# Optimization experiments

Hardware: AMD Instinct MI355X
Metric: run time of the kernel (lower is better)

The kernel has to match this reference:

```python
import jax, jax.numpy as jnp
import numpy as np

# PQMatcher forward (cleaned): per passage timestep i, additive (Bahdanau-style)
# attention over all question positions:
#   x = tanh(Wp(Up[i]) + Wq(Uq) + Wv(v));  s = x . v;  a = softmax(s over lq)
#   c[i] = a @ Uq
# The original python loop over i is loop-invariant except Wp(Up[i]), so it
# vectorizes exactly into one broadcasted tanh + einsum. (The original also
# computed a duplicate s_/a_ from Upr==Up and Uqr==Uq which is identical math
# and unused; we compute it once.)

LP, LQ, BZ, SZ, H = 400, 50, 32, 768, 128


def setup_inputs() -> dict:
    key = jax.random.key(0)
    ks = jax.random.split(key, 9)
    s_in = 1.0 / np.sqrt(SZ)
    s_h = 1.0 / np.sqrt(H)
    return {
        "Up": jax.random.normal(ks[0], (LP, BZ, SZ), jnp.float32),
        "Uq": jax.random.normal(ks[1], (LQ, BZ, SZ), jnp.float32),
        "Wp_w": jax.random.normal(ks[2], (H, SZ), jnp.float32) * s_in,
        "Wp_b": jax.random.normal(ks[3], (H,), jnp.float32) * s_in,
        "Wq_w": jax.random.normal(ks[4], (H, SZ), jnp.float32) * s_in,
        "Wq_b": jax.random.normal(ks[5], (H,), jnp.float32) * s_in,
        "Wv_w": jax.random.normal(ks[6], (H, H), jnp.float32) * s_h,
        "Wv_b": jax.random.normal(ks[7], (H,), jnp.float32) * s_h,
        "v": jax.random.normal(ks[8], (BZ, H), jnp.float32),
    }


def reference(Up, Uq, Wp_w, Wp_b, Wq_w, Wq_b, Wv_w, Wv_b, v):
    # Projections (loop-invariant parts hoisted out of the original loop)
    Wup = jnp.einsum("pbs,hs->pbh", Up, Wp_w) + Wp_b  # [lp, bz, h]
    Wuq = jnp.einsum("qbs,hs->qbh", Uq, Wq_w) + Wq_b  # [lq, bz, h]
    Wvv = jnp.einsum("bh,gh->bg", v, Wv_w) + Wv_b      # [bz, h]
    # tanh score fusion: [lp, lq, bz, h]
    x = jnp.tanh(Wup[:, None, :, :] + Wuq[None, :, :, :] + Wvv[None, None, :, :])
    # scores s[i] = x[i] . v  -> [lp, bz, lq]
    s = jnp.einsum("pqbh,bh->pbq", x, v)
    a = jax.nn.softmax(s, axis=-1)                      # softmax over question len
    # contexts c[i] = a[i] @ Uq -> [lp, bz, sz]
    c = jnp.einsum("pbq,qbs->pbs", a, Uq)
    return c
```

## Files before the change

### kernel.cpp

```cpp
#include <hip/hip_runtime.h>

#define LP 400
#define LQ 50
#define BZ 32
#define SZ 768
#define HH 128
#define PR_TOT 14400

typedef unsigned short u16;
typedef __attribute__((ext_vector_type(8))) short short8;
typedef __attribute__((ext_vector_type(4))) float f32x4;

__device__ __forceinline__ float fexp2(float x) {
#if __has_builtin(__builtin_amdgcn_exp2f)
  return __builtin_amdgcn_exp2f(x);
#else
  return exp2f(x);
#endif
}
__device__ __forceinline__ float frcp(float x) {
#if __has_builtin(__builtin_amdgcn_rcpf)
  return __builtin_amdgcn_rcpf(x);
#else
  return 1.0f / x;
#endif
}

__device__ __forceinline__ unsigned pack2(float x, float y) {
  return (__float_as_uint(x) >> 16) | (__float_as_uint(y) & 0xffff0000u);
}
__device__ __forceinline__ float remf(float x) {
  return x - __uint_as_float(__float_as_uint(x) & 0xffff0000u);
}

__global__ __launch_bounds__(256) void prep_kernel(
    const float* __restrict__ Wp_w, const float* __restrict__ Wq_w,
    const float* __restrict__ v, const float* __restrict__ Wv_w,
    const float* __restrict__ Wv_b,
    u16* __restrict__ Wph, u16* __restrict__ Wpl,
    u16* __restrict__ Wqh, u16* __restrict__ Wql, float* __restrict__ Wvv) {
  const int bx = blockIdx.x, t = threadIdx.x;
  if (bx < 96) {
    int gid = bx * 256 + t;
    int base = gid * 8;
    const float* src;
    u16 *dh, *dl;
    if (base < HH * SZ) {
      src = Wp_w + base; dh = Wph + base; dl = Wpl + base;
    } else {
      int o = base - HH * SZ;
      src = Wq_w + o; dh = Wqh + o; dl = Wql + o;
    }
    float4 x0 = *(const float4*)src;
    float4 x1 = *(const float4*)(src + 4);
    uint4 H, L;
    H.x = pack2(x0.x, x0.y); H.y = pack2(x0.z, x0.w);
    H.z = pack2(x1.x, x1.y); H.w = pack2(x1.z, x1.w);
    L.x = pack2(remf(x0.x), remf(x0.y)); L.y = pack2(remf(x0.z), remf(x0.w));
    L.z = pack2(remf(x1.x), remf(x1.y)); L.w = pack2(remf(x1.z), remf(x1.w));
    *(uint4*)dh = H;
    *(uint4*)dl = L;
  } else {
    int id = (bx - 96) * 256 + t;
    int b = id >> 7, g = id & 127;
    const float4* vb = reinterpret_cast<const float4*>(v + b * HH);
    const float4* wr = reinterpret_cast<const float4*>(Wv_w + g * HH);
    float s = Wv_b[g];
#pragma unroll
    for (int i = 0; i < HH / 4; ++i) {
      float4 a = vb[i], w = wr[i];
      s = fmaf(a.x, w.x, s); s = fmaf(a.y, w.y, s);
      s = fmaf(a.z, w.z, s); s = fmaf(a.w, w.w, s);
    }
    Wvv[id] = s;
  }
}

__global__ __launch_bounds__(256, 2) void mfma_gemm(
    const float* __restrict__ Up, const float* __restrict__ Uq,
    const u16* __restrict__ Wph, const u16* __restrict__ Wpl,
    const u16* __restrict__ Wqh, const u16* __restrict__ Wql,
    float* __restrict__ partial) {
  __shared__ u16 Ah[64][40], Al[64][40], Bh[128][40], Bl[128][40];
  const int t = threadIdx.x, lane = t & 63, wid = t >> 6;
  const int bx = blockIdx.x, z = blockIdx.y;
  const int m0 = bx * 64;
  const bool probq = (bx >= 200);
  const u16* WH = probq ? Wqh : Wph;
  const u16* WL = probq ? Wql : Wpl;
  const int k0base = z * 384;

  const int ra = t >> 1, kh = (t & 1) * 16;
  const bool hasA = (ra < 64);
  const int grow = m0 + (ra & 63);
  const float* srcA = (grow < 12800) ? (Up + (size_t)grow * SZ)
                                     : (Uq + (size_t)(grow - 12800) * SZ);
  const u16* srcWH = WH + ra * SZ;
  const u16* srcWL = WL + ra * SZ;

  const int wm = (wid >> 1) * 32, wn = (wid & 1) * 64;
  const int fr = lane & 15, fg = lane >> 4;

  f32x4 acc[2][4];
#pragma unroll
  for (int i = 0; i < 2; ++i)
#pragma unroll
    for (int j = 0; j < 4; ++j) acc[i][j] = (f32x4){0.f, 0.f, 0.f, 0.f};

  float4 a0, a1, a2, a3;
  uint4 wh0, wh1, wl0, wl1;

#define GLOAD(s)                                                         \
  do {                                                                   \
    int kk = k0base + (s) * 32 + kh;                                     \
    if (hasA) {                                                          \
      a0 = *(const float4*)(srcA + kk);                                  \
      a1 = *(const float4*)(srcA + kk + 4);                              \
      a2 = *(const float4*)(srcA + kk + 8);                              \
      a3 = *(const float4*)(srcA + kk + 12);                             \
    }                                                                    \
    wh0 = *(const uint4*)(srcWH + kk); wh1 = *(const uint4*)(srcWH + kk + 8); \
    wl0 = *(const uint4*)(srcWL + kk); wl1 = *(const uint4*)(srcWL + kk + 8); \
  } while (0)

#define WSTORE()                                                          \
  do {                                                                    \
    if (hasA) {                                                           \
      uint4 H0, H1, L0, L1;                                               \
      H0.x = pack2(a0.x, a0.y); H0.y = pack2(a0.z, a0.w);                 \
      H0.z = pack2(a1.x, a1.y); H0.w = pack2(a1.z, a1.w);                 \
      H1.x = pack2(a2.x, a2.y); H1.y = pack2(a2.z, a2.w);                 \
      H1.z = pack2(a3.x, a3.y); H1.w = pack2(a3.z, a3.w);                 \
      L0.x = pack2(remf(a0.x), remf(a0.y)); L0.y = pack2(remf(a0.z), remf(a0.w)); \
      L0.z = pack2(remf(a1.x), remf(a1.y)); L0.w = pack2(remf(a1.z), remf(a1.w)); \
      L1.x = pack2(remf(a2.x), remf(a2.y)); L1.y = pack2(remf(a2.z), remf(a2.w)); \
      L1.z = pack2(remf(a3.x), remf(a3.y)); L1.w = pack2(remf(a3.z), remf(a3.w)); \
      *(uint4*)&Ah[ra][kh] = H0; *(uint4*)&Ah[ra][kh + 8] = H1;           \
      *(uint4*)&Al[ra][kh] = L0; *(uint4*)&Al[ra][kh + 8] = L1;           \
    }                                                                     \
    *(uint4*)&Bh[ra][kh] = wh0; *(uint4*)&Bh[ra][kh + 8] = wh1;           \
    *(uint4*)&Bl[ra][kh] = wl0; *(uint4*)&Bl[ra][kh + 8] = wl1;           \
  } while (0)

  GLOAD(0);
  WSTORE();
  __syncthreads();

  for (int s = 0; s < 12; ++s) {
    if (s < 11) GLOAD(s + 1);
    short8 ah[2], al[2], bh[4], bl[4];
#pragma unroll
    for (int i = 0; i < 2; ++i) {
      ah[i] = *(const short8*)&Ah[wm + i * 16 + fr][fg * 8];
      al[i] = *(const short8*)&Al[wm + i * 16 + fr][fg * 8];
    }
#pragma unroll
    for (int j = 0; j < 4; ++j) {
      bh[j] = *(const short8*)&Bh[wn + j * 16 + fr][fg * 8];
      bl[j] = *(const short8*)&Bl[wn + j * 16 + fr][fg * 8];
    }
#pragma unroll
    for (int i = 0; i < 2; ++i)
#pragma unroll
      for (int j = 0; j < 4; ++j) {
        acc[i][j] = __builtin_amdgcn_mfma_f32_16x16x32_bf16(ah[i], bh[j], acc[i][j], 0, 0, 0);
        acc[i][j] = __builtin_amdgcn_mfma_f32_16x16x32_bf16(ah[i], bl[j], acc[i][j], 0, 0, 0);
        acc[i][j] = __builtin_amdgcn_mfma_f32_16x16x32_bf16(al[i], bh[j], acc[i][j], 0, 0, 0);
      }
    __syncthreads();
    if (s < 11) WSTORE();
    __syncthreads();
  }
#undef GLOAD
#undef WSTORE

  float* pz = partial + (size_t)z * (PR_TOT * HH);
#pragma unroll
  for (int i = 0; i < 2; ++i) {
    int r0 = m0 + wm + i * 16 + fg * 4;
#pragma unroll
    for (int j = 0; j < 4; ++j) {
      int c = wn + j * 16 + fr;
#pragma unroll
      for (int e = 0; e < 4; ++e) pz[(size_t)(r0 + e) * HH + c] = acc[i][j][e];
    }
  }
}

__global__ __launch_bounds__(256, 4) void score_ctx(
    const float* __restrict__ partial, const float* __restrict__ Wp_b,
    const float* __restrict__ Wq_b, const float* __restrict__ Wvv,
    const float* __restrict__ v, const float* __restrict__ Uq,
    float* __restrict__ out, float TS) {
  const int f = blockIdx.x;
  const int b = ((f & 7) << 2) | ((f >> 3) & 3);
  const int pbase = (f >> 5) * 8;
  const int t = threadIdx.x, lane = t & 63, w = t >> 6;
  __shared__ float W2s[HH][52];
  __shared__ f32x4 Wps4[8][32];
  __shared__ f32x4 vsh4[32];
  __shared__ float as_[8][52];

  for (int ff = t; ff < LQ * 32; ff += 256) {
    int q_ = ff % LQ, c4 = ff / LQ;
    size_t row = 12800 + (size_t)(q_ * BZ + b);
    float4 p0 = *(const float4*)&partial[row * HH + c4 * 4];
    float4 p1 = *(const float4*)&partial[((size_t)PR_TOT + row) * HH + c4 * 4];
    float4 bb = *(const float4*)&Wq_b[c4 * 4];
    float4 wv = *(const float4*)&Wvv[b * HH + c4 * 4];
    W2s[c4 * 4 + 0][q_] = (p0.x + p1.x + bb.x + wv.x) * TS;
    W2s[c4 * 4 + 1][q_] = (p0.y + p1.y + bb.y + wv.y) * TS;
    W2s[c4 * 4 + 2][q_] = (p0.z + p1.z + bb.z + wv.z) * TS;
    W2s[c4 * 4 + 3][q_] = (p0.w + p1.w + bb.w + wv.w) * TS;
  }
  {
    int i = t >> 5, c4 = t & 31;
    size_t grow = (size_t)(pbase + i) * BZ + b;
    float4 p0 = *(const float4*)&partial[grow * HH + c4 * 4];
    float4 p1 = *(const float4*)&partial[((size_t)PR_TOT + grow) * HH + c4 * 4];
    float4 bb = *(const float4*)&Wp_b[c4 * 4];
    Wps4[i][c4] = (f32x4){(p0.x + p1.x + bb.x) * TS, (p0.y + p1.y + bb.y) * TS,
                          (p0.z + p1.z + bb.z) * TS, (p0.w + p1.w + bb.w) * TS};
  }
  if (t < 32) {
    float4 x = *(const float4*)&v[b * HH + t * 4];
    vsh4[t] = (f32x4){x.x, x.y, x.z, x.w};
  }
  __syncthreads();

  const int q = (lane < LQ) ? lane : (LQ - 1);
  const int prow = w * 2;
  float A0 = 0.f, A1 = 0.f;
  for (int h4 = 0; h4 < 32; ++h4) {
    f32x4 vj = vsh4[h4];
    f32x4 w0 = Wps4[prow][h4];
    f32x4 w1 = Wps4[prow + 1][h4];
    float s0 = W2s[h4 * 4 + 0][q];
    float s1 = W2s[h4 * 4 + 1][q];
    float s2 = W2s[h4 * 4 + 2][q];
    float s3 = W2s[h4 * 4 + 3][q];
    A0 = fmaf(vj[0], frcp(fexp2(w0[0] + s0) + 1.f), A0);
    A0 = fmaf(vj[1], frcp(fexp2(w0[1] + s1) + 1.f), A0);
    A0 = fmaf(vj[2], frcp(fexp2(w0[2] + s2) + 1.f), A0);
    A0 = fmaf(vj[3], frcp(fexp2(w0[3] + s3) + 1.f), A0);
    A1 = fmaf(vj[0], frcp(fexp2(w1[0] + s0) + 1.f), A1);
    A1 = fmaf(vj[1], frcp(fexp2(w1[1] + s1) + 1.f), A1);
    A1 = fmaf(vj[2], frcp(fexp2(w1[2] + s2) + 1.f), A1);
    A1 = fmaf(vj[3], frcp(fexp2(w1[3] + s3) + 1.f), A1);
  }

#define SOFTMAX(AR, PI)                                                   \
  do {                                                                    \
    float a = (lane < LQ) ? (AR) : 1e30f;                                 \
    float mn = a;                                                         \
    mn = fminf(mn, __shfl_xor(mn, 1));  mn = fminf(mn, __shfl_xor(mn, 2)); \
    mn = fminf(mn, __shfl_xor(mn, 4));  mn = fminf(mn, __shfl_xor(mn, 8)); \
    mn = fminf(mn, __shfl_xor(mn, 16)); mn = fminf(mn, __shfl_xor(mn, 32)); \
    float e = fexp2((mn - a) * TS);         \
    float sm = e;                                                         \
    sm += __shfl_xor(sm, 1);  sm += __shfl_xor(sm, 2);                    \
    sm += __shfl_xor(sm, 4);  sm += __shfl_xor(sm, 8);                    \
    sm += __shfl_xor(sm, 16); sm += __shfl_xor(sm, 32);                   \
    float val = e * frcp(sm);                                             \
    if (lane < LQ) as_[prow + (PI)][lane] = val;                          \
  } while (0)

  SOFTMAX(A0, 0); SOFTMAX(A1, 1);
#undef SOFTMAX
  __syncthreads();

  if (t < 192) {
    const int s4 = t * 4;
    f32x4 acc[8];
#pragma unroll
    for (int i = 0; i < 8; ++i) acc[i] = (f32x4){0.f, 0.f, 0.f, 0.f};
    for (int qp = 0; qp < LQ; qp += 2) {
      float4 u0 = *(const float4*)&Uq[(size_t)(qp * BZ + b) * SZ + s4];
      float4 u1 = *(const float4*)&Uq[(size_t)((qp + 1) * BZ + b) * SZ + s4];
#pragma unroll
      for (int i = 0; i < 8; ++i) {
        float2 a2 = *(const float2*)&as_[i][qp];
        acc[i][0] = fmaf(a2.x, u0.x, acc[i][0]); acc[i][1] = fmaf(a2.x, u0.y, acc[i][1]);
        acc[i][2] = fmaf(a2.x, u0.z, acc[i][2]); acc[i][3] = fmaf(a2.x, u0.w, acc[i][3]);
        acc[i][0] = fmaf(a2.y, u1.x, acc[i][0]); acc[i][1] = fmaf(a2.y, u1.y, acc[i][1]);
        acc[i][2] = fmaf(a2.y, u1.z, acc[i][2]); acc[i][3] = fmaf(a2.y, u1.w, acc[i][3]);
      }
    }
#pragma unroll
    for (int i = 0; i < 8; ++i) {
      float4 r = make_float4(acc[i][0], acc[i][1], acc[i][2], acc[i][3]);
      *(float4*)&out[(size_t)((pbase + i) * BZ + b) * SZ + s4] = r;
    }
  }
}

extern "C" void kernel_launch(void* const* d_in, const int* in_sizes, int n_in,
                              void* d_out, int out_size, void* d_ws, size_t ws_size,
                              hipStream_t stream) {
  const float* Up   = (const float*)d_in[0];
  const float* Uq   = (const float*)d_in[1];
  const float* Wp_w = (const float*)d_in[2];
  const float* Wp_b = (const float*)d_in[3];
  const float* Wq_w = (const float*)d_in[4];
  const float* Wq_b = (const float*)d_in[5];
  const float* Wv_w = (const float*)d_in[6];
  const float* Wv_b = (const float*)d_in[7];
  const float* v    = (const float*)d_in[8];
  float* out = (float*)d_out;

  float* ws      = (float*)d_ws;
  float* Wvv     = ws;
  u16* Wph       = (u16*)(Wvv + BZ * HH);
  u16* Wpl       = Wph + HH * SZ;
  u16* Wqh       = Wpl + HH * SZ;
  u16* Wql       = Wqh + HH * SZ;
  float* partial = (float*)(Wql + HH * SZ);

  const float TS = 2.8853900817779268f;

  prep_kernel<<<dim3(112), dim3(256), 0, stream>>>(
      Wp_w, Wq_w, v, Wv_w, Wv_b, Wph, Wpl, Wqh, Wql, Wvv);
  mfma_gemm<<<dim3(225, 2), dim3(256), 0, stream>>>(
      Up, Uq, Wph, Wpl, Wqh, Wql, partial);
  score_ctx<<<dim3(1600), dim3(256), 0, stream>>>(
      partial, Wp_b, Wq_b, Wvv, v, Uq, out, TS);
}
```

Baseline: 174.3 us.

## Split GEMM K four ways and separate score and context kernels

Raises the split-K factor of the projection GEMM from 2 to 4, so twice as many blocks each run half as many K steps. The fused score/context kernel is split into a score+softmax kernel that writes attention weights to workspace and a separate 192-thread context kernel. Each block now handles 16 passage rows instead of 8, with a b-major mapping chosen per XCD to improve reuse of the Uq and partial rows. In exchange it writes and reads twice as many partial sums, adds a global round trip for the attention weights, and costs one more kernel launch.

Result: slower. 313.1 us (+79.7%).

```diff
diff --git a/kernel.cpp b/kernel.cpp
--- a/kernel.cpp
+++ b/kernel.cpp
@@ -6,6 +6,7 @@
 #define SZ 768
 #define HH 128
 #define PR_TOT 14400
+#define NZ 4
 
 typedef unsigned short u16;
 typedef __attribute__((ext_vector_type(8))) short short8;
@@ -88,7 +89,7 @@
   const bool probq = (bx >= 200);
   const u16* WH = probq ? Wqh : Wph;
   const u16* WL = probq ? Wql : Wpl;
-  const int k0base = z * 384;
+  const int k0base = z * 192;
 
   const int ra = t >> 1, kh = (t & 1) * 16;
   const bool hasA = (ra < 64);
@@ -146,8 +147,8 @@
   WSTORE();
   __syncthreads();
 
-  for (int s = 0; s < 12; ++s) {
-    if (s < 11) GLOAD(s + 1);
+  for (int s = 0; s < 6; ++s) {
+    if (s < 5) GLOAD(s + 1);
     short8 ah[2], al[2], bh[4], bl[4];
 #pragma unroll
     for (int i = 0; i < 2; ++i) {
@@ -168,7 +169,7 @@
         acc[i][j] = __builtin_amdgcn_mfma_f32_16x16x32_bf16(al[i], bh[j], acc[i][j], 0, 0, 0);
       }
     __syncthreads();
-    if (s < 11) WSTORE();
+    if (s < 5) WSTORE();
     __syncthreads();
   }
 #undef GLOAD
@@ -187,40 +188,49 @@
   }
 }
 
-__global__ __launch_bounds__(256, 4) void score_ctx(
+__global__ __launch_bounds__(256, 4) void score_kernel(
     const float* __restrict__ partial, const float* __restrict__ Wp_b,
     const float* __restrict__ Wq_b, const float* __restrict__ Wvv,
-    const float* __restrict__ v, const float* __restrict__ Uq,
-    float* __restrict__ out, float TS) {
+    const float* __restrict__ v, float* __restrict__ aw, float TS) {
   const int f = blockIdx.x;
-  const int b = ((f & 7) << 2) | ((f >> 3) & 3);
-  const int pbase = (f >> 5) * 8;
+  const int xcd = f & 7, j = f >> 3;
+  const int b = xcd * 4 + j / 25;
+  const int pbase = (j % 25) * 16;
   const int t = threadIdx.x, lane = t & 63, w = t >> 6;
   __shared__ float W2s[HH][52];
-  __shared__ f32x4 Wps4[8][32];
+  __shared__ f32x4 Wps4[16][32];
   __shared__ f32x4 vsh4[32];
-  __shared__ float as_[8][52];
 
   for (int ff = t; ff < LQ * 32; ff += 256) {
     int q_ = ff % LQ, c4 = ff / LQ;
     size_t row = 12800 + (size_t)(q_ * BZ + b);
-    float4 p0 = *(const float4*)&partial[row * HH + c4 * 4];
-    float4 p1 = *(const float4*)&partial[((size_t)PR_TOT + row) * HH + c4 * 4];
+    const float* pp = &partial[row * HH + c4 * 4];
+    float4 p0 = *(const float4*)pp;
+    float4 p1 = *(const float4*)(pp + (size_t)PR_TOT * HH);
+    float4 p2 = *(const float4*)(pp + (size_t)2 * PR_TOT * HH);
+    float4 p3 = *(const float4*)(pp + (size_t)3 * PR_TOT * HH);
     float4 bb = *(const float4*)&Wq_b[c4 * 4];
     float4 wv = *(const float4*)&Wvv[b * HH + c4 * 4];
-    W2s[c4 * 4 + 0][q_] = (p0.x + p1.x + bb.x + wv.x) * TS;
-    W2s[c4 * 4 + 1][q_] = (p0.y + p1.y + bb.y + wv.y) * TS;
-    W2s[c4 * 4 + 2][q_] = (p0.z + p1.z + bb.z + wv.z) * TS;
-    W2s[c4 * 4 + 3][q_] = (p0.w + p1.w + bb.w + wv.w) * TS;
-  }
-  {
-    int i = t >> 5, c4 = t & 31;
+    W2s[c4 * 4 + 0][q_] = (p0.x + p1.x + p2.x + p3.x + bb.x + wv.x) * TS;
+    W2s[c4 * 4 + 1][q_] = (p0.y + p1.y + p2.y + p3.y + bb.y + wv.y) * TS;
+    W2s[c4 * 4 + 2][q_] = (p0.z + p1.z + p2.z + p3.z + bb.z + wv.z) * TS;
+    W2s[c4 * 4 + 3][q_] = (p0.w + p1.w + p2.w + p3.w + bb.w + wv.w) * TS;
+  }
+#pragma unroll
+  for (int rep = 0; rep < 2; ++rep) {
+    int ff = t + rep * 256;
+    int i = ff >> 5, c4 = ff & 31;
     size_t grow = (size_t)(pbase + i) * BZ + b;
-    float4 p0 = *(const float4*)&partial[grow * HH + c4 * 4];
-    float4 p1 = *(const float4*)&partial[((size_t)PR_TOT + grow) * HH + c4 * 4];
+    const float* pp = &partial[grow * HH + c4 * 4];
+    float4 p0 = *(const float4*)pp;
+    float4 p1 = *(const float4*)(pp + (size_t)PR_TOT * HH);
+    float4 p2 = *(const float4*)(pp + (size_t)2 * PR_TOT * HH);
+    float4 p3 = *(const float4*)(pp + (size_t)3 * PR_TOT * HH);
     float4 bb = *(const float4*)&Wp_b[c4 * 4];
-    Wps4[i][c4] = (f32x4){(p0.x + p1.x + bb.x) * TS, (p0.y + p1.y + bb.y) * TS,
-                          (p0.z + p1.z + bb.z) * TS, (p0.w + p1.w + bb.w) * TS};
+    Wps4[i][c4] = (f32x4){(p0.x + p1.x + p2.x + p3.x + bb.x) * TS,
+                          (p0.y + p1.y + p2.y + p3.y + bb.y) * TS,
+                          (p0.z + p1.z + p2.z + p3.z + bb.z) * TS,
+                          (p0.w + p1.w + p2.w + p3.w + bb.w) * TS};
   }
   if (t < 32) {
     float4 x = *(const float4*)&v[b * HH + t * 4];
@@ -229,12 +239,14 @@
   __syncthreads();
 
   const int q = (lane < LQ) ? lane : (LQ - 1);
-  const int prow = w * 2;
-  float A0 = 0.f, A1 = 0.f;
+  const int prow = w * 4;
+  float A0 = 0.f, A1 = 0.f, A2 = 0.f, A3 = 0.f;
   for (int h4 = 0; h4 < 32; ++h4) {
     f32x4 vj = vsh4[h4];
-    f32x4 w0 = Wps4[prow][h4];
+    f32x4 w0 = Wps4[prow + 0][h4];
     f32x4 w1 = Wps4[prow + 1][h4];
+    f32x4 w2 = Wps4[prow + 2][h4];
+    f32x4 w3 = Wps4[prow + 3][h4];
     float s0 = W2s[h4 * 4 + 0][q];
     float s1 = W2s[h4 * 4 + 1][q];
     float s2 = W2s[h4 * 4 + 2][q];
@@ -247,6 +259,14 @@
     A1 = fmaf(vj[1], frcp(fexp2(w1[1] + s1) + 1.f), A1);
     A1 = fmaf(vj[2], frcp(fexp2(w1[2] + s2) + 1.f), A1);
     A1 = fmaf(vj[3], frcp(fexp2(w1[3] + s3) + 1.f), A1);
+    A2 = fmaf(vj[0], frcp(fexp2(w2[0] + s0) + 1.f), A2);
+    A2 = fmaf(vj[1], frcp(fexp2(w2[1] + s1) + 1.f), A2);
+    A2 = fmaf(vj[2], frcp(fexp2(w2[2] + s2) + 1.f), A2);
+    A2 = fmaf(vj[3], frcp(fexp2(w2[3] + s3) + 1.f), A2);
+    A3 = fmaf(vj[0], frcp(fexp2(w3[0] + s0) + 1.f), A3);
+    A3 = fmaf(vj[1], frcp(fexp2(w3[1] + s1) + 1.f), A3);
+    A3 = fmaf(vj[2], frcp(fexp2(w3[2] + s2) + 1.f), A3);
+    A3 = fmaf(vj[3], frcp(fexp2(w3[3] + s3) + 1.f), A3);
   }
 
 #define SOFTMAX(AR, PI)                                                   \
@@ -262,35 +282,48 @@
     sm += __shfl_xor(sm, 4);  sm += __shfl_xor(sm, 8);                    \
     sm += __shfl_xor(sm, 16); sm += __shfl_xor(sm, 32);                   \
     float val = e * frcp(sm);                                             \
-    if (lane < LQ) as_[prow + (PI)][lane] = val;                          \
+    if (lane < LQ)                                                        \
+      aw[(size_t)((pbase + prow + (PI)) * BZ + b) * LQ + lane] = val;     \
   } while (0)
 
-  SOFTMAX(A0, 0); SOFTMAX(A1, 1);
+  SOFTMAX(A0, 0); SOFTMAX(A1, 1); SOFTMAX(A2, 2); SOFTMAX(A3, 3);
 #undef SOFTMAX
+}
+
+__global__ __launch_bounds__(192, 5) void ctx_kernel(
+    const float* __restrict__ aw, const float* __restrict__ Uq,
+    float* __restrict__ out) {
+  const int f = blockIdx.x;
+  const int xcd = f & 7, j = f >> 3;
+  const int b = xcd * 4 + j / 25;
+  const int pbase = (j % 25) * 16;
+  const int t = threadIdx.x;
+  __shared__ float as_[16][52];
+  for (int ff = t; ff < 16 * LQ; ff += 192) {
+    int i = ff / LQ, qq = ff - i * LQ;
+    as_[i][qq] = aw[(size_t)((pbase + i) * BZ + b) * LQ + qq];
+  }
   __syncthreads();
-
-  if (t < 192) {
-    const int s4 = t * 4;
-    f32x4 acc[8];
-#pragma unroll
-    for (int i = 0; i < 8; ++i) acc[i] = (f32x4){0.f, 0.f, 0.f, 0.f};
-    for (int qp = 0; qp < LQ; qp += 2) {
-      float4 u0 = *(const float4*)&Uq[(size_t)(qp * BZ + b) * SZ + s4];
-      float4 u1 = *(const float4*)&Uq[(size_t)((qp + 1) * BZ + b) * SZ + s4];
-#pragma unroll
-      for (int i = 0; i < 8; ++i) {
-        float2 a2 = *(const float2*)&as_[i][qp];
-        acc[i][0] = fmaf(a2.x, u0.x, acc[i][0]); acc[i][1] = fmaf(a2.x, u0.y, acc[i][1]);
-        acc[i][2] = fmaf(a2.x, u0.z, acc[i][2]); acc[i][3] = fmaf(a2.x, u0.w, acc[i][3]);
-        acc[i][0] = fmaf(a2.y, u1.x, acc[i][0]); acc[i][1] = fmaf(a2.y, u1.y, acc[i][1]);
-        acc[i][2] = fmaf(a2.y, u1.z, acc[i][2]); acc[i][3] = fmaf(a2.y, u1.w, acc[i][3]);
-      }
-    }
-#pragma unroll
-    for (int i = 0; i < 8; ++i) {
-      float4 r = make_float4(acc[i][0], acc[i][1], acc[i][2], acc[i][3]);
-      *(float4*)&out[(size_t)((pbase + i) * BZ + b) * SZ + s4] = r;
-    }
+  const int s4 = t * 4;
+  f32x4 acc[16];
+#pragma unroll
+  for (int i = 0; i < 16; ++i) acc[i] = (f32x4){0.f, 0.f, 0.f, 0.f};
+  for (int qp = 0; qp < LQ; qp += 2) {
+    float4 u0 = *(const float4*)&Uq[(size_t)(qp * BZ + b) * SZ + s4];
+    float4 u1 = *(const float4*)&Uq[(size_t)((qp + 1) * BZ + b) * SZ + s4];
+#pragma unroll
+    for (int i = 0; i < 16; ++i) {
+      float2 a2 = *(const float2*)&as_[i][qp];
+      acc[i][0] = fmaf(a2.x, u0.x, acc[i][0]); acc[i][1] = fmaf(a2.x, u0.y, acc[i][1]);
+      acc[i][2] = fmaf(a2.x, u0.z, acc[i][2]); acc[i][3] = fmaf(a2.x, u0.w, acc[i][3]);
+      acc[i][0] = fmaf(a2.y, u1.x, acc[i][0]); acc[i][1] = fmaf(a2.y, u1.y, acc[i][1]);
+      acc[i][2] = fmaf(a2.y, u1.z, acc[i][2]); acc[i][3] = fmaf(a2.y, u1.w, acc[i][3]);
+    }
+  }
+#pragma unroll
+  for (int i = 0; i < 16; ++i) {
+    float4 r = make_float4(acc[i][0], acc[i][1], acc[i][2], acc[i][3]);
+    *(float4*)&out[(size_t)((pbase + i) * BZ + b) * SZ + s4] = r;
   }
 }
 
@@ -310,7 +343,8 @@
 
   float* ws      = (float*)d_ws;
   float* Wvv     = ws;
-  u16* Wph       = (u16*)(Wvv + BZ * HH);
+  float* aw      = Wvv + BZ * HH;
+  u16* Wph       = (u16*)(aw + LP * BZ * LQ);
   u16* Wpl       = Wph + HH * SZ;
   u16* Wqh       = Wpl + HH * SZ;
   u16* Wql       = Wqh + HH * SZ;
@@ -320,8 +354,9 @@
 
   prep_kernel<<<dim3(112), dim3(256), 0, stream>>>(
       Wp_w, Wq_w, v, Wv_w, Wv_b, Wph, Wpl, Wqh, Wql, Wvv);
-  mfma_gemm<<<dim3(225, 2), dim3(256), 0, stream>>>(
+  mfma_gemm<<<dim3(225, NZ), dim3(256), 0, stream>>>(
       Up, Uq, Wph, Wpl, Wqh, Wql, partial);
-  score_ctx<<<dim3(1600), dim3(256), 0, stream>>>(
-      partial, Wp_b, Wq_b, Wvv, v, Uq, out, TS);
-}
+  score_kernel<<<dim3(800), dim3(256), 0, stream>>>(
+      partial, Wp_b, Wq_b, Wvv, v, aw, TS);
+  ctx_kernel<<<dim3(800), dim3(192), 0, stream>>>(aw, Uq, out);
+}
```
